# Kernel tuning notes

Hardware: AMD Instinct MI355X
Metric: run time of the kernel (lower is better)

Reference implementation:

```python
import jax, jax.numpy as jnp
import numpy as np

N = 50000
E = 800000
IN_DIM, HID, LAT, DEC_HID = 256, 256, 128, 512


def _glorot(key, shape):
    fan_in, fan_out = shape
    lim = np.sqrt(6.0 / (fan_in + fan_out))
    return jax.random.uniform(key, shape, jnp.float32, -lim, lim)


def setup_inputs() -> dict:
    key = jax.random.key(0)
    ks = jax.random.split(key, 10)
    x = jax.random.normal(ks[0], (N, IN_DIM), jnp.float32)
    edge_index = jax.random.randint(ks[1], (2, E), 0, N, dtype=jnp.int64)
    return {
        "x": x,
        "edge_index": edge_index,
        "W1": _glorot(ks[2], (IN_DIM, HID)), "b1": jnp.zeros((HID,), jnp.float32),
        "W2": _glorot(ks[3], (HID, LAT)), "b2": jnp.zeros((LAT,), jnp.float32),
        "Wd1": _glorot(ks[4], (LAT, DEC_HID)), "bd1": jnp.zeros((DEC_HID,), jnp.float32),
        "Wd2": _glorot(ks[5], (DEC_HID, IN_DIM)), "bd2": jnp.zeros((IN_DIM,), jnp.float32),
    }


def _gcn_layer(x, src, dst, W, b, num_nodes):
    # linear transform
    xt = x @ W + b                      # [N, out]
    # scatter-mean aggregation over incoming edges (PyG aggr='mean')
    msg = xt[src]                       # [E, out] gather of source features
    summed = jax.ops.segment_sum(msg, dst, num_segments=num_nodes)
    cnt = jax.ops.segment_sum(jnp.ones((src.shape[0],), xt.dtype), dst,
                              num_segments=num_nodes)
    mean = summed / jnp.maximum(cnt, 1.0)[:, None]   # 0 for isolated nodes
    # relu + residual
    return jax.nn.relu(mean) + xt


def reference(x, edge_index, W1, b1, W2, b2, Wd1, bd1, Wd2, bd2):
    src, dst = edge_index[0], edge_index[1]
    h = _gcn_layer(x, src, dst, W1, b1, x.shape[0])
    z = _gcn_layer(h, src, dst, W2, b2, x.shape[0])
    # decoder MLP
    x_hat = jax.nn.relu(z @ Wd1 + bd1) @ Wd2 + bd2
    return (x_hat, z)
```

## Files before the change

kernel.cpp:

```cpp
#include <hip/hip_runtime.h>
#include <hip/hip_bf16.h>

#define TPB 256

typedef __attribute__((ext_vector_type(8))) short short8;
typedef __attribute__((ext_vector_type(4))) float f32x4;

__device__ __forceinline__ unsigned short f2bf(float f) {
    unsigned int u = __float_as_uint(f);
    u = (u + 0x7FFFu + ((u >> 16) & 1u)) >> 16;
    return (unsigned short)u;
}
__device__ __forceinline__ float bflo(unsigned int u) { return __uint_as_float(u << 16); }
__device__ __forceinline__ float bfhi(unsigned int u) { return __uint_as_float(u & 0xFFFF0000u); }

__device__ __forceinline__ void gload16(const void* g, void* l) {
    __builtin_amdgcn_global_load_lds(
        (const __attribute__((address_space(1))) unsigned int*)g,
        (__attribute__((address_space(3))) unsigned int*)l, 16, 0, 0);
}

__global__ void transpose_convert_all(
    const float* __restrict__ Wa, unsigned short* __restrict__ Ta, int Ka, int Na,
    const float* __restrict__ Wb, unsigned short* __restrict__ Tb, int Kb, int Nb,
    const float* __restrict__ Wc, unsigned short* __restrict__ Tc, int Kc, int Nc_,
    const float* __restrict__ Wd, unsigned short* __restrict__ Td, int Kd, int Nd)
{
    __shared__ float tile[32][33];
    int b = blockIdx.x;
    const float* W; unsigned short* T; int K, Nn;
    const int ta = (Na / 32) * (Ka / 32);
    const int tb = (Nb / 32) * (Kb / 32);
    const int tc = (Nc_ / 32) * (Kc / 32);
    if (b < ta)                { W = Wa; T = Ta; K = Ka; Nn = Na; }
    else if (b < ta + tb)      { b -= ta;           W = Wb; T = Tb; K = Kb; Nn = Nb; }
    else if (b < ta + tb + tc) { b -= ta + tb;      W = Wc; T = Tc; K = Kc; Nn = Nc_; }
    else                       { b -= ta + tb + tc; W = Wd; T = Td; K = Kd; Nn = Nd; }
    const int nx = Nn / 32;
    const int n0 = (b % nx) * 32;
    const int k0 = (b / nx) * 32;
    const int tx = threadIdx.x, ty = threadIdx.y;
#pragma unroll
    for (int i = 0; i < 4; ++i)
        tile[ty + i * 8][tx] = W[(size_t)(k0 + ty + i * 8) * Nn + n0 + tx];
    __syncthreads();
#pragma unroll
    for (int i = 0; i < 4; ++i)
        T[(size_t)(n0 + ty + i * 8) * K + k0 + tx] = f2bf(tile[tx][ty + i * 8]);
}

__device__ __forceinline__ void load_a16f(const float* p, short8& lo, short8& hi) {
    float4 f0 = *reinterpret_cast<const float4*>(p);
    float4 f1 = *reinterpret_cast<const float4*>(p + 4);
    float4 f2 = *reinterpret_cast<const float4*>(p + 8);
    float4 f3 = *reinterpret_cast<const float4*>(p + 12);
    lo[0] = (short)f2bf(f0.x); lo[1] = (short)f2bf(f0.y);
    lo[2] = (short)f2bf(f0.z); lo[3] = (short)f2bf(f0.w);
    lo[4] = (short)f2bf(f1.x); lo[5] = (short)f2bf(f1.y);
    lo[6] = (short)f2bf(f1.z); lo[7] = (short)f2bf(f1.w);
    hi[0] = (short)f2bf(f2.x); hi[1] = (short)f2bf(f2.y);
    hi[2] = (short)f2bf(f2.z); hi[3] = (short)f2bf(f2.w);
    hi[4] = (short)f2bf(f3.x); hi[5] = (short)f2bf(f3.y);
    hi[6] = (short)f2bf(f3.z); hi[7] = (short)f2bf(f3.w);
}

__device__ __forceinline__ void copy_out32(unsigned short* C, const float* Cst, const float* bias,
                                           int rowbase, int bn, int M, int Nc, int t, bool doRelu) {
#pragma unroll
    for (int it = 0; it < 2; ++it) {
        const int idx = it * 2048 + t * 8;
        const int row = idx >> 7, col = idx & 127;
        const int m = rowbase + row;
        if (m >= M) continue;
        float4 v0 = *reinterpret_cast<const float4*>(&Cst[idx]);
        float4 v1 = *reinterpret_cast<const float4*>(&Cst[idx + 4]);
        float4 b0 = *reinterpret_cast<const float4*>(&bias[bn + col]);
        float4 b1 = *reinterpret_cast<const float4*>(&bias[bn + col + 4]);
        float o[8] = {v0.x + b0.x, v0.y + b0.y, v0.z + b0.z, v0.w + b0.w,
                      v1.x + b1.x, v1.y + b1.y, v1.z + b1.z, v1.w + b1.w};
        short8 s;
#pragma unroll
        for (int j = 0; j < 8; ++j) {
            const float vv = doRelu ? fmaxf(o[j], 0.f) : o[j];
            s[j] = (short)f2bf(vv);
        }
        *reinterpret_cast<short8*>(&C[(size_t)m * Nc + bn + col]) = s;
    }
}
__device__ __forceinline__ void copy_out32(float* C, const float* Cst, const float* bias,
                                           int rowbase, int bn, int M, int Nc, int t, bool doRelu) {
#pragma unroll
    for (int it = 0; it < 4; ++it) {
        const int idx = it * 1024 + t * 4;
        const int row = idx >> 7, col = idx & 127;
        const int m = rowbase + row;
        if (m >= M) continue;
        float4 v = *reinterpret_cast<const float4*>(&Cst[idx]);
        float4 b = *reinterpret_cast<const float4*>(&bias[bn + col]);
        v.x += b.x; v.y += b.y; v.z += b.z; v.w += b.w;
        if (doRelu) {
            v.x = fmaxf(v.x, 0.f); v.y = fmaxf(v.y, 0.f);
            v.z = fmaxf(v.z, 0.f); v.w = fmaxf(v.w, 0.f);
        }
        *reinterpret_cast<float4*>(&C[(size_t)m * Nc + bn + col]) = v;
    }
}

template <typename TA, typename TC, int K, bool RELU>
__global__ __launch_bounds__(256) void mfma_gemm4(
    const TA* __restrict__ A, const unsigned short* __restrict__ Bt,
    const float* __restrict__ bias, TC* __restrict__ C, int M, int Nc)
{
    __shared__ unsigned short lds_s[2][12288];
    constexpr bool AF32 = (sizeof(TA) == 4);

    const int t  = threadIdx.x;
    const int l  = t & 63;
    const int w  = t >> 6;
    const int wm = w >> 1, wn = w & 1;
    const int bm = blockIdx.x * 64;
    const int bn = blockIdx.y * 128;

    f32x4 acc[2][4] = {};

    const int r4 = t >> 2;
    const int q4 = t & 3;
    const int gmr = bm + r4;
    short8 sa0, sa1;

    auto loadAregs = [&](int k0) {
        if (gmr < M) load_a16f((const float*)A + (size_t)gmr * K + k0 + q4 * 16, sa0, sa1);
        else { sa0 = (short8)0; sa1 = (short8)0; }
    };
    auto writeAregs = [&](int buf) {
        const int s0 = (2 * q4)     ^ (r4 & 7);
        const int s1 = (2 * q4 + 1) ^ (r4 & 7);
        *reinterpret_cast<short8*>(&lds_s[buf][r4 * 64 + s0 * 8]) = sa0;
        *reinterpret_cast<short8*>(&lds_s[buf][r4 * 64 + s1 * 8]) = sa1;
    };
    auto stageA_lds = [&](int buf, int k0) {
#pragma unroll
        for (int ii = 0; ii < 2; ++ii) {
            const int seg = w + ii * 4;
            const int rr  = seg * 8 + (l >> 3);
            const int ss  = l & 7;
            const int gr  = min(bm + rr, M - 1);
            gload16((const unsigned short*)A + (size_t)gr * K + k0 + ((ss ^ (rr & 7)) * 8),
                    &lds_s[buf][seg * 512]);
        }
    };
    auto stageB = [&](int buf, int k0) {
#pragma unroll
        for (int ii = 0; ii < 4; ++ii) {
            const int seg = w + ii * 4;
            const int rr  = seg * 8 + (l >> 3);
            const int ss  = l & 7;
            gload16(Bt + (size_t)(bn + rr) * K + k0 + ((ss ^ (rr & 7)) * 8),
                    &lds_s[buf][4096 + seg * 512]);
        }
    };

    constexpr int S = K / 64;

    if (AF32) {
        loadAregs(0);
        writeAregs(0);
        if (S > 1) loadAregs(64);
    } else {
        stageA_lds(0, 0);
    }
    stageB(0, 0);
    __syncthreads();

#pragma unroll
    for (int step = 0; step < S; ++step) {
        const int k0  = step * 64;
        const int cur = step & 1;

        if (step + 1 < S) {
            if (AF32) writeAregs(cur ^ 1);
            else      stageA_lds(cur ^ 1, k0 + 64);
            stageB(cur ^ 1, k0 + 64);
        }
        if (AF32 && step + 2 < S) loadAregs(k0 + 128);

#pragma unroll
        for (int kk = 0; kk < 2; ++kk) {
            short8 af[2], bf4[4];
#pragma unroll
            for (int mf = 0; mf < 2; ++mf) {
                const int row  = wm * 32 + mf * 16 + (l & 15);
                const int slot = (kk * 4 + (l >> 4)) ^ (row & 7);
                af[mf] = *reinterpret_cast<const short8*>(&lds_s[cur][row * 64 + slot * 8]);
            }
#pragma unroll
            for (int nf = 0; nf < 4; ++nf) {
                const int row  = wn * 64 + nf * 16 + (l & 15);
                const int slot = (kk * 4 + (l >> 4)) ^ (row & 7);
                bf4[nf] = *reinterpret_cast<const short8*>(&lds_s[cur][4096 + row * 64 + slot * 8]);
            }
#pragma unroll
            for (int mf = 0; mf < 2; ++mf)
#pragma unroll
                for (int nf = 0; nf < 4; ++nf)
                    acc[mf][nf] = __builtin_amdgcn_mfma_f32_16x16x32_bf16(
                        af[mf], bf4[nf], acc[mf][nf], 0, 0, 0);
        }
        __syncthreads();
    }

    float* Cst = reinterpret_cast<float*>(lds_s);
#pragma unroll
    for (int p = 0; p < 2; ++p) {
        if (wm == p) {
#pragma unroll
            for (int mf = 0; mf < 2; ++mf)
#pragma unroll
                for (int nf = 0; nf < 4; ++nf)
#pragma unroll
                    for (int rr = 0; rr < 4; ++rr) {
                        const int row = mf * 16 + (l >> 4) * 4 + rr;
                        const int col = wn * 64 + nf * 16 + (l & 15);
                        Cst[row * 128 + col] = acc[mf][nf][rr];
                    }
        }
        __syncthreads();
        copy_out32(C, Cst, bias, bm + p * 32, bn, M, Nc, t, RELU);
        if (p == 0) __syncthreads();
    }
}

__global__ __launch_bounds__(256) void fused_decoder(
    const unsigned short* __restrict__ Z,
    const unsigned short* __restrict__ Wt1,
    const float* __restrict__ b1v,
    const unsigned short* __restrict__ Wt2,
    const float* __restrict__ b2v,
    float* __restrict__ Xh, int M)
{
    __shared__ unsigned short z_s[4096];
    __shared__ unsigned short hd_s[16384];
    __shared__ unsigned short b_s[16384];

    const int t = threadIdx.x;
    const int l = t & 63;
    const int w = t >> 6;
    const int bm = blockIdx.x * 32;

#pragma unroll
    for (int ii = 0; ii < 2; ++ii) {
        const int seg = w + ii * 4;
        const int r   = seg * 4 + (l >> 4);
        const int sl  = l & 15;
        const int gr  = min(bm + r, M - 1);
        gload16(Z + (size_t)gr * 128 + ((sl ^ (r & 15)) * 8), &z_s[seg * 512]);
    }

    auto stageB = [&](const unsigned short* W, int Krow, int rowbase, int k0) {
#pragma unroll
        for (int ii = 0; ii < 8; ++ii) {
            const int seg = w + ii * 4;
            const int rr  = seg * 8 + (l >> 3);
            const int sl  = l & 7;
            gload16(W + (size_t)(rowbase + rr) * Krow + k0 + ((sl ^ (rr & 7)) * 8),
                    &b_s[seg * 512]);
        }
    };

    f32x4 acc[2][4];

#pragma unroll
    for (int p = 0; p < 4; ++p) {
        const int nc = p >> 1, st = p & 1;
        stageB(Wt1, 128, nc * 256, st * 64);
        __syncthreads();
        if (st == 0) {
#pragma unroll
            for (int mf = 0; mf < 2; ++mf)
#pragma unroll
                for (int nf = 0; nf < 4; ++nf) acc[mf][nf] = (f32x4)(0.f);
        }
#pragma unroll
        for (int kk = 0; kk < 2; ++kk) {
            const int kc  = st * 8 + kk * 4 + (l >> 4);
            const int kc2 = kk * 4 + (l >> 4);
            short8 af[2], bf[4];
#pragma unroll
            for (int mf = 0; mf < 2; ++mf) {
                const int r = mf * 16 + (l & 15);
                af[mf] = *reinterpret_cast<const short8*>(&z_s[r * 128 + ((kc ^ (r & 15)) * 8)]);
            }
#pragma unroll
            for (int nf = 0; nf < 4; ++nf) {
                const int r = w * 64 + nf * 16 + (l & 15);
                bf[nf] = *reinterpret_cast<const short8*>(&b_s[r * 64 + ((kc2 ^ (r & 7)) * 8)]);
            }
#pragma unroll
            for (int mf = 0; mf < 2; ++mf)
#pragma unroll
                for (int nf = 0; nf < 4; ++nf)
                    acc[mf][nf] = __builtin_amdgcn_mfma_f32_16x16x32_bf16(
                        af[mf], bf[nf], acc[mf][nf], 0, 0, 0);
        }
        if (st == 1) {
#pragma unroll
            for (int mf = 0; mf < 2; ++mf)
#pragma unroll
                for (int nf = 0; nf < 4; ++nf) {
                    const int c  = nc * 256 + w * 64 + nf * 16 + (l & 15);
                    const float bv = b1v[c];
#pragma unroll
                    for (int rr = 0; rr < 4; ++rr) {
                        const int r = mf * 16 + (l >> 4) * 4 + rr;
                        const float v = fmaxf(acc[mf][nf][rr] + bv, 0.f);
                        hd_s[r * 512 + (((c >> 3) ^ (r & 7)) * 8) + (c & 7)] = f2bf(v);
                    }
                }
        }
        __syncthreads();
    }

#pragma unroll
    for (int mf = 0; mf < 2; ++mf)
#pragma unroll
        for (int nf = 0; nf < 4; ++nf) acc[mf][nf] = (f32x4)(0.f);

    for (int step = 0; step < 8; ++step) {
        stageB(Wt2, 512, 0, step * 64);
        __syncthreads();
#pragma unroll
        for (int kk = 0; kk < 2; ++kk) {
            const int kc  = step * 8 + kk * 4 + (l >> 4);
            const int kc2 = kk * 4 + (l >> 4);
            short8 af[2], bf[4];
#pragma unroll
            for (int mf = 0; mf < 2; ++mf) {
                const int r = mf * 16 + (l & 15);
                af[mf] = *reinterpret_cast<const short8*>(&hd_s[r * 512 + ((kc ^ (r & 7)) * 8)]);
            }
#pragma unroll
            for (int nf = 0; nf < 4; ++nf) {
                const int r = w * 64 + nf * 16 + (l & 15);
                bf[nf] = *reinterpret_cast<const short8*>(&b_s[r * 64 + ((kc2 ^ (r & 7)) * 8)]);
            }
#pragma unroll
            for (int mf = 0; mf < 2; ++mf)
#pragma unroll
                for (int nf = 0; nf < 4; ++nf)
                    acc[mf][nf] = __builtin_amdgcn_mfma_f32_16x16x32_bf16(
                        af[mf], bf[nf], acc[mf][nf], 0, 0, 0);
        }
        __syncthreads();
    }

    float* Cst = reinterpret_cast<float*>(b_s);
#pragma unroll
    for (int mf = 0; mf < 2; ++mf)
#pragma unroll
        for (int nf = 0; nf < 4; ++nf)
#pragma unroll
            for (int rr = 0; rr < 4; ++rr) {
                const int r = mf * 16 + (l >> 4) * 4 + rr;
                const int c = w * 64 + nf * 16 + (l & 15);
                Cst[r * 256 + c] = acc[mf][nf][rr];
            }
    __syncthreads();
#pragma unroll
    for (int it = 0; it < 8; ++it) {
        const int idx = it * 1024 + t * 4;
        const int r = idx >> 8, c = idx & 255;
        if (bm + r < M) {
            float4 v = *reinterpret_cast<const float4*>(&Cst[idx]);
            float4 b = *reinterpret_cast<const float4*>(&b2v[c]);
            v.x += b.x; v.y += b.y; v.z += b.z; v.w += b.w;
            *reinterpret_cast<float4*>(&Xh[(size_t)(bm + r) * 256 + c]) = v;
        }
    }
}

__global__ void hist_kernel(const int* __restrict__ dst, int* __restrict__ counts,
                            int E, int csz)
{
    const int chunk = blockIdx.x & 7;
    const int blk   = blockIdx.x >> 3;
    const int lo = chunk * csz, hi = lo + csz;
    const int base = (blk * TPB + threadIdx.x) * 4;
    if (base + 3 < E) {
        int4 d4 = *reinterpret_cast<const int4*>(dst + base);
        if (d4.x >= lo && d4.x < hi) atomicAdd(&counts[d4.x], 1);
        if (d4.y >= lo && d4.y < hi) atomicAdd(&counts[d4.y], 1);
        if (d4.z >= lo && d4.z < hi) atomicAdd(&counts[d4.z], 1);
        if (d4.w >= lo && d4.w < hi) atomicAdd(&counts[d4.w], 1);
    } else {
        for (int e = base; e < E; ++e) {
            const int d = dst[e];
            if (d >= lo && d < hi) atomicAdd(&counts[d], 1);
        }
    }
}

__global__ void scan1_kernel(const int* __restrict__ counts,
                             int* __restrict__ local, int* __restrict__ bsum, int N)
{
    __shared__ int sh[TPB];
    const int t = threadIdx.x;
    const int base = blockIdx.x * 1024 + t * 4;
    int v[4];
#pragma unroll
    for (int i = 0; i < 4; ++i) v[i] = (base + i < N) ? counts[base + i] : 0;
    const int s = v[0] + v[1] + v[2] + v[3];
    sh[t] = s;
    __syncthreads();
    for (int d = 1; d < TPB; d <<= 1) {
        int x = (t >= d) ? sh[t - d] : 0;
        __syncthreads();
        sh[t] += x;
        __syncthreads();
    }
    int run = sh[t] - s;
#pragma unroll
    for (int i = 0; i < 4; ++i) {
        if (base + i < N) local[base + i] = run;
        run += v[i];
    }
    if (t == TPB - 1) bsum[blockIdx.x] = sh[TPB - 1];
}

__global__ void scan2_kernel(int* __restrict__ bsum, int nb)
{
    __shared__ int sh[TPB];
    const int t = threadIdx.x;
    const int v = (t < nb) ? bsum[t] : 0;
    sh[t] = v;
    __syncthreads();
    for (int d = 1; d < TPB; d <<= 1) {
        int x = (t >= d) ? sh[t - d] : 0;
        __syncthreads();
        sh[t] += x;
        __syncthreads();
    }
    if (t < nb) bsum[t] = sh[t] - v;
}

__global__ void scan3_kernel(int* __restrict__ offsets, int* __restrict__ cursor,
                             const int* __restrict__ bsum, int N)
{
    const int i = blockIdx.x * TPB + threadIdx.x;
    if (i < N) {
        const int o = offsets[i] + bsum[i >> 10];
        offsets[i] = o;
        cursor[i]  = o;
    }
}

__global__ void build_perm_kernel(const int* __restrict__ src, const int* __restrict__ dst,
                                  int* __restrict__ cursor, int* __restrict__ perm,
                                  int E, int csz)
{
    const int chunk = blockIdx.x & 7;
    const int blk   = blockIdx.x >> 3;
    const int lo = chunk * csz, hi = lo + csz;
    const int base = (blk * TPB + threadIdx.x) * 4;
    if (base + 3 < E) {
        int4 d4 = *reinterpret_cast<const int4*>(dst + base);
        if (d4.x >= lo && d4.x < hi) { int p = atomicAdd(&cursor[d4.x], 1); perm[p] = src[base + 0]; }
        if (d4.y >= lo && d4.y < hi) { int p = atomicAdd(&cursor[d4.y], 1); perm[p] = src[base + 1]; }
        if (d4.z >= lo && d4.z < hi) { int p = atomicAdd(&cursor[d4.z], 1); perm[p] = src[base + 2]; }
        if (d4.w >= lo && d4.w < hi) { int p = atomicAdd(&cursor[d4.w], 1); perm[p] = src[base + 3]; }
    } else {
        for (int e = base; e < E; ++e) {
            const int d = dst[e];
            if (d >= lo && d < hi) { int p = atomicAdd(&cursor[d], 1); perm[p] = src[e]; }
        }
    }
}

template <int F, int CH, bool WRITE_ZF32>
__global__ __launch_bounds__(256) void agg_kernel(
    const uint2* __restrict__ xt,
    const int* __restrict__ offsets, const int* __restrict__ counts,
    const int* __restrict__ perm,
    uint2* __restrict__ out, float* __restrict__ zf32, int N)
{
    constexpr int RU  = F / 4;
    constexpr int L   = RU / CH;
    constexpr int NPB = TPB / L;

    const int chunk = blockIdx.x % CH;
    const int node  = (blockIdx.x / CH) * NPB + threadIdx.x / L;
    const int g     = threadIdx.x % L;
    if (node >= N) return;
    const int col = chunk * L + g;

    const int start = offsets[node];
    const int deg   = counts[node];

    float a0 = 0.f, a1 = 0.f, a2 = 0.f, a3 = 0.f;

    for (int base = 0; base < deg; base += L) {
        const int m = min(L, deg - base);
        const int pidx = perm[start + base + ((g < m) ? g : (m - 1))];
        int j = 0;
        for (; j + 4 <= m; j += 4) {
            const int s0 = __shfl(pidx, j + 0, L);
            const int s1 = __shfl(pidx, j + 1, L);
            const int s2 = __shfl(pidx, j + 2, L);
            const int s3 = __shfl(pidx, j + 3, L);
            const uint2 v0 = xt[(size_t)s0 * RU + col];
            const uint2 v1 = xt[(size_t)s1 * RU + col];
            const uint2 v2 = xt[(size_t)s2 * RU + col];
            const uint2 v3 = xt[(size_t)s3 * RU + col];
            a0 += bflo(v0.x) + bflo(v1.x) + bflo(v2.x) + bflo(v3.x);
            a1 += bfhi(v0.x) + bfhi(v1.x) + bfhi(v2.x) + bfhi(v3.x);
            a2 += bflo(v0.y) + bflo(v1.y) + bflo(v2.y) + bflo(v3.y);
            a3 += bfhi(v0.y) + bfhi(v1.y) + bfhi(v2.y) + bfhi(v3.y);
        }
        for (; j < m; ++j) {
            const int s = __shfl(pidx, j, L);
            const uint2 v = xt[(size_t)s * RU + col];
            a0 += bflo(v.x); a1 += bfhi(v.x);
            a2 += bflo(v.y); a3 += bfhi(v.y);
        }
    }

    const float c = (float)max(deg, 1);
    const uint2 xv = xt[(size_t)node * RU + col];
    const float r0 = fmaxf(a0 / c, 0.f) + bflo(xv.x);
    const float r1 = fmaxf(a1 / c, 0.f) + bfhi(xv.x);
    const float r2 = fmaxf(a2 / c, 0.f) + bflo(xv.y);
    const float r3 = fmaxf(a3 / c, 0.f) + bfhi(xv.y);

    uint2 o;
    o.x = (unsigned int)f2bf(r0) | ((unsigned int)f2bf(r1) << 16);
    o.y = (unsigned int)f2bf(r2) | ((unsigned int)f2bf(r3) << 16);
    out[(size_t)node * RU + col] = o;
    if (WRITE_ZF32) {
        float4 z4 = make_float4(r0, r1, r2, r3);
        *reinterpret_cast<float4*>(&zf32[(size_t)node * F + 4 * col]) = z4;
    }
}

extern "C" void kernel_launch(void* const* d_in, const int* in_sizes, int n_in,
                              void* d_out, int out_size, void* d_ws, size_t ws_size,
                              hipStream_t stream)
{
    const int IN_DIM = 256, HID = 256, LAT = 128, DEC_HID = 512;
    const int N = in_sizes[0] / IN_DIM;
    const int E = in_sizes[1] / 2;

    const float* x   = (const float*)d_in[0];
    const int*   ei  = (const int*)d_in[1];
    const float* W1  = (const float*)d_in[2];
    const float* b1  = (const float*)d_in[3];
    const float* W2  = (const float*)d_in[4];
    const float* b2  = (const float*)d_in[5];
    const float* Wd1 = (const float*)d_in[6];
    const float* bd1 = (const float*)d_in[7];
    const float* Wd2 = (const float*)d_in[8];
    const float* bd2 = (const float*)d_in[9];

    const int* src = ei;
    const int* dst = ei + E;

    unsigned short* xt1  = (unsigned short*)d_ws;
    unsigned short* h    = xt1  + (size_t)N * 256;
    unsigned short* xt2  = h    + (size_t)N * 256;
    unsigned short* zbf  = xt2  + (size_t)N * 128;
    unsigned short* hdec = zbf  + (size_t)N * 128;
    unsigned short* wt1  = hdec + (size_t)N * 512;
    unsigned short* wt2  = wt1  + 256 * 256;
    unsigned short* wtd1 = wt2  + 128 * 256;
    unsigned short* wtd2 = wtd1 + 512 * 128;
    int* counts  = (int*)(wtd2 + 256 * 512);
    int* offsets = counts + N;
    int* cursor  = offsets + N;
    int* bsum    = cursor + N;
    int* perm    = bsum + 256;

    float* out_xhat = (float*)d_out;
    float* out_z    = out_xhat + (size_t)N * IN_DIM;

    dim3 blk(TPB);
    const int mb64 = (N + 63) / 64;
    const int nscan = (N + 1023) / 1024;
    const int csz = (N + 7) / 8;
    const int egrid8 = ((E + TPB * 4 - 1) / (TPB * 4)) * 8;

    {
        const int tiles = (HID/32)*(IN_DIM/32) + (LAT/32)*(HID/32)
                        + (DEC_HID/32)*(LAT/32) + (IN_DIM/32)*(DEC_HID/32);
        transpose_convert_all<<<tiles, dim3(32, 8), 0, stream>>>(
            W1, wt1, IN_DIM, HID,  W2, wt2, HID, LAT,
            Wd1, wtd1, LAT, DEC_HID,  Wd2, wtd2, DEC_HID, IN_DIM);
    }

    hipMemsetAsync(counts, 0, (size_t)N * 4, stream);
    hist_kernel<<<egrid8, blk, 0, stream>>>(dst, counts, E, csz);
    scan1_kernel<<<nscan, blk, 0, stream>>>(counts, offsets, bsum, N);
    scan2_kernel<<<1, blk, 0, stream>>>(bsum, nscan);
    scan3_kernel<<<(N + TPB - 1) / TPB, blk, 0, stream>>>(offsets, cursor, bsum, N);
    build_perm_kernel<<<egrid8, blk, 0, stream>>>(src, dst, cursor, perm, E, csz);

    mfma_gemm4<float, unsigned short, 256, false><<<dim3(mb64, HID / 128), blk, 0, stream>>>(
        x, wt1, b1, xt1, N, HID);
    {
        const int ngroups = (N + 15) / 16;
        agg_kernel<256, 4, false><<<ngroups * 4, blk, 0, stream>>>(
            (const uint2*)xt1, offsets, counts, perm, (uint2*)h, nullptr, N);
    }

    mfma_gemm4<unsigned short, unsigned short, 256, false><<<dim3(mb64, LAT / 128), blk, 0, stream>>>(
        h, wt2, b2, xt2, N, LAT);
    {
        const int ngroups = (N + 15) / 16;
        agg_kernel<128, 2, true><<<ngroups * 2, blk, 0, stream>>>(
            (const uint2*)xt2, offsets, counts, perm, (uint2*)zbf, out_z, N);
    }

    fused_decoder<<<(N + 31) / 32, blk, 0, stream>>>(
        zbf, wtd1, bd1, wtd2, bd2, out_xhat, N);
}
```

Measured before the change: 267.0 us.

## Read decoder weights directly from global memory instead of staging through LDS

The fused decoder no longer stages weight tiles into a 32KB shared buffer. Each wave now loads its B fragments straight from global memory (relying on L2 caching of the small weight matrices), which removes the per-step barriers and the staging buffer. Lower LDS use plus launch_bounds(256,4) aim to raise occupancy. The risk is uncoalesced or high-latency global loads in the inner MFMA loop. The now-unused hdec workspace buffer is also dropped.

After: 302.0 us. +13.1%, slower.

```diff
diff --git a/kernel.cpp b/kernel.cpp
--- a/kernel.cpp
+++ b/kernel.cpp
@@ -230,7 +230,7 @@
     }
 }
 
-__global__ __launch_bounds__(256) void fused_decoder(
+__global__ __launch_bounds__(256, 4) void fused_decoder(
     const unsigned short* __restrict__ Z,
     const unsigned short* __restrict__ Wt1,
     const float* __restrict__ b1v,
@@ -240,7 +240,6 @@
 {
     __shared__ unsigned short z_s[4096];
     __shared__ unsigned short hd_s[16384];
-    __shared__ unsigned short b_s[16384];
 
     const int t = threadIdx.x;
     const int l = t & 63;
@@ -255,105 +254,83 @@
         const int gr  = min(bm + r, M - 1);
         gload16(Z + (size_t)gr * 128 + ((sl ^ (r & 15)) * 8), &z_s[seg * 512]);
     }
-
-    auto stageB = [&](const unsigned short* W, int Krow, int rowbase, int k0) {
-#pragma unroll
-        for (int ii = 0; ii < 8; ++ii) {
-            const int seg = w + ii * 4;
-            const int rr  = seg * 8 + (l >> 3);
-            const int sl  = l & 7;
-            gload16(W + (size_t)(rowbase + rr) * Krow + k0 + ((sl ^ (rr & 7)) * 8),
-                    &b_s[seg * 512]);
-        }
-    };
-
-    f32x4 acc[2][4];
-
-#pragma unroll
-    for (int p = 0; p < 4; ++p) {
-        const int nc = p >> 1, st = p & 1;
-        stageB(Wt1, 128, nc * 256, st * 64);
-        __syncthreads();
-        if (st == 0) {
-#pragma unroll
-            for (int mf = 0; mf < 2; ++mf)
-#pragma unroll
-                for (int nf = 0; nf < 4; ++nf) acc[mf][nf] = (f32x4)(0.f);
-        }
+    __syncthreads();
+
+#pragma unroll
+    for (int nc = 0; nc < 2; ++nc) {
+        f32x4 acc[2][4] = {};
+#pragma unroll
+        for (int st = 0; st < 2; ++st) {
+#pragma unroll
+            for (int kk = 0; kk < 2; ++kk) {
+                const int kc = st * 8 + kk * 4 + (l >> 4);
+                short8 af[2], bf[4];
+#pragma unroll
+                for (int mf = 0; mf < 2; ++mf) {
+                    const int r = mf * 16 + (l & 15);
+                    af[mf] = *reinterpret_cast<const short8*>(
+                        &z_s[r * 128 + ((kc ^ (r & 15)) * 8)]);
+                }
+#pragma unroll
+                for (int nf = 0; nf < 4; ++nf) {
+                    const int row = nc * 256 + w * 64 + nf * 16 + (l & 15);
+                    bf[nf] = *reinterpret_cast<const short8*>(
+                        Wt1 + (size_t)row * 128 + st * 64 + (kk * 4 + (l >> 4)) * 8);
+                }
+#pragma unroll
+                for (int mf = 0; mf < 2; ++mf)
+#pragma unroll
+                    for (int nf = 0; nf < 4; ++nf)
+                        acc[mf][nf] = __builtin_amdgcn_mfma_f32_16x16x32_bf16(
+                            af[mf], bf[nf], acc[mf][nf], 0, 0, 0);
+            }
+        }
+#pragma unroll
+        for (int mf = 0; mf < 2; ++mf)
+#pragma unroll
+            for (int nf = 0; nf < 4; ++nf) {
+                const int c  = nc * 256 + w * 64 + nf * 16 + (l & 15);
+                const float bv = b1v[c];
+#pragma unroll
+                for (int rr = 0; rr < 4; ++rr) {
+                    const int r = mf * 16 + (l >> 4) * 4 + rr;
+                    const float v = fmaxf(acc[mf][nf][rr] + bv, 0.f);
+                    hd_s[r * 512 + (((c >> 3) ^ (r & 7)) * 8) + (c & 7)] = f2bf(v);
+                }
+            }
+    }
+    __syncthreads();
+
+    f32x4 acc2[2][4] = {};
+#pragma unroll
+    for (int step = 0; step < 8; ++step) {
 #pragma unroll
         for (int kk = 0; kk < 2; ++kk) {
-            const int kc  = st * 8 + kk * 4 + (l >> 4);
-            const int kc2 = kk * 4 + (l >> 4);
+            const int kc = step * 8 + kk * 4 + (l >> 4);
             short8 af[2], bf[4];
 #pragma unroll
             for (int mf = 0; mf < 2; ++mf) {
                 const int r = mf * 16 + (l & 15);
-                af[mf] = *reinterpret_cast<const short8*>(&z_s[r * 128 + ((kc ^ (r & 15)) * 8)]);
+                af[mf] = *reinterpret_cast<const short8*>(
+                    &hd_s[r * 512 + ((kc ^ (r & 7)) * 8)]);
             }
 #pragma unroll
             for (int nf = 0; nf < 4; ++nf) {
-                const int r = w * 64 + nf * 16 + (l & 15);
-                bf[nf] = *reinterpret_cast<const short8*>(&b_s[r * 64 + ((kc2 ^ (r & 7)) * 8)]);
+                const int row = w * 64 + nf * 16 + (l & 15);
+                bf[nf] = *reinterpret_cast<const short8*>(
+                    Wt2 + (size_t)row * 512 + step * 64 + (kk * 4 + (l >> 4)) * 8);
             }
 #pragma unroll
             for (int mf = 0; mf < 2; ++mf)
 #pragma unroll
                 for (int nf = 0; nf < 4; ++nf)
-                    acc[mf][nf] = __builtin_amdgcn_mfma_f32_16x16x32_bf16(
-                        af[mf], bf[nf], acc[mf][nf], 0, 0, 0);
-        }
-        if (st == 1) {
-#pragma unroll
-            for (int mf = 0; mf < 2; ++mf)
-#pragma unroll
-                for (int nf = 0; nf < 4; ++nf) {
-                    const int c  = nc * 256 + w * 64 + nf * 16 + (l & 15);
-                    const float bv = b1v[c];
-#pragma unroll
-                    for (int rr = 0; rr < 4; ++rr) {
-                        const int r = mf * 16 + (l >> 4) * 4 + rr;
-                        const float v = fmaxf(acc[mf][nf][rr] + bv, 0.f);
-                        hd_s[r * 512 + (((c >> 3) ^ (r & 7)) * 8) + (c & 7)] = f2bf(v);
-                    }
-                }
-        }
-        __syncthreads();
-    }
-
-#pragma unroll
-    for (int mf = 0; mf < 2; ++mf)
-#pragma unroll
-        for (int nf = 0; nf < 4; ++nf) acc[mf][nf] = (f32x4)(0.f);
-
-    for (int step = 0; step < 8; ++step) {
-        stageB(Wt2, 512, 0, step * 64);
-        __syncthreads();
-#pragma unroll
-        for (int kk = 0; kk < 2; ++kk) {
-            const int kc  = step * 8 + kk * 4 + (l >> 4);
-            const int kc2 = kk * 4 + (l >> 4);
-            short8 af[2], bf[4];
-#pragma unroll
-            for (int mf = 0; mf < 2; ++mf) {
-                const int r = mf * 16 + (l & 15);
-                af[mf] = *reinterpret_cast<const short8*>(&hd_s[r * 512 + ((kc ^ (r & 7)) * 8)]);
-            }
-#pragma unroll
-            for (int nf = 0; nf < 4; ++nf) {
-                const int r = w * 64 + nf * 16 + (l & 15);
-                bf[nf] = *reinterpret_cast<const short8*>(&b_s[r * 64 + ((kc2 ^ (r & 7)) * 8)]);
-            }
-#pragma unroll
-            for (int mf = 0; mf < 2; ++mf)
-#pragma unroll
-                for (int nf = 0; nf < 4; ++nf)
-                    acc[mf][nf] = __builtin_amdgcn_mfma_f32_16x16x32_bf16(
-                        af[mf], bf[nf], acc[mf][nf], 0, 0, 0);
-        }
-        __syncthreads();
-    }
-
-    float* Cst = reinterpret_cast<float*>(b_s);
+                    acc2[mf][nf] = __builtin_amdgcn_mfma_f32_16x16x32_bf16(
+                        af[mf], bf[nf], acc2[mf][nf], 0, 0, 0);
+        }
+    }
+    __syncthreads();
+
+    float* Cst = reinterpret_cast<float*>(hd_s);
 #pragma unroll
     for (int mf = 0; mf < 2; ++mf)
 #pragma unroll
@@ -362,7 +339,7 @@
             for (int rr = 0; rr < 4; ++rr) {
                 const int r = mf * 16 + (l >> 4) * 4 + rr;
                 const int c = w * 64 + nf * 16 + (l & 15);
-                Cst[r * 256 + c] = acc[mf][nf][rr];
+                Cst[r * 256 + c] = acc2[mf][nf][rr];
             }
     __syncthreads();
 #pragma unroll
@@ -566,8 +543,7 @@
     unsigned short* h    = xt1  + (size_t)N * 256;
     unsigned short* xt2  = h    + (size_t)N * 256;
     unsigned short* zbf  = xt2  + (size_t)N * 128;
-    unsigned short* hdec = zbf  + (size_t)N * 128;
-    unsigned short* wt1  = hdec + (size_t)N * 512;
+    unsigned short* wt1  = zbf  + (size_t)N * 128;
     unsigned short* wt2  = wt1  + 256 * 256;
     unsigned short* wtd1 = wt2  + 128 * 256;
     unsigned short* wtd2 = wtd1 + 512 * 128;
```
